# Optimization experiments

Hardware: AMD Instinct MI355X
Metric: run time of the kernel (lower is better)

The kernel has to match this reference:

```python
import jax, jax.numpy as jnp
import numpy as np
from jax import lax

KS = 5            # patch kernel size
STRIDE = 4        # patch stride / scale ratio
SHIFTS = (2, 2)   # roll shifts before patch extraction
SOFTMAX_SCALE = 10.0
MID_CH = 64
BAND_HS = 8


def same_pad(x, k, s):
    """TensorFlow-style SAME padding for kernel k, stride s (NCHW)."""
    H, W = x.shape[-2], x.shape[-1]
    oh, ow = -(-H // s), -(-W // s)
    ph = max(0, (oh - 1) * s + k - H)
    pw = max(0, (ow - 1) * s + k - W)
    return jnp.pad(x, ((0, 0), (0, 0), (ph // 2, ph - ph // 2), (pw // 2, pw - pw // 2)))


def extract_patches(x, k, s, shifts):
    """torch.nn.Unfold equivalent with SAME padding and roll -> [N, L, C, k, k]."""
    x = same_pad(x, k, s)
    x = jnp.roll(x, shifts[0], axis=2)
    x = jnp.roll(x, shifts[1], axis=3)
    p = lax.conv_general_dilated_patches(
        x, (k, k), (s, s), 'VALID', dimension_numbers=('NCHW', 'OIHW', 'NCHW'))
    N, _, Hn, Wn = p.shape
    C = x.shape[1]
    # channel ordering is (C, kh, kw) channel-slowest, matching torch unfold
    return p.reshape(N, C, k, k, Hn * Wn).transpose(0, 4, 1, 2, 3)


def conv3(x, w, b):
    """3x3 conv, padding=1, bias + LeakyReLU(0.01) (BasicBlock)."""
    y = lax.conv_general_dilated(x, w, (1, 1), [(1, 1), (1, 1)],
                                 dimension_numbers=('NCHW', 'OIHW', 'NCHW'))
    return jax.nn.leaky_relu(y + b[None, :, None, None], 0.01)


def setup_inputs() -> dict:
    key = jax.random.key(0)
    ks = jax.random.split(key, 11)
    f32 = jnp.float32
    return {
        'ms':   jax.random.normal(ks[0], (2, BAND_HS, 96, 96), f32),
        'pan':  jax.random.normal(ks[1], (2, 1, 384, 384), f32),
        'pan2': jax.random.normal(ks[2], (2, 1, 96, 96), f32),
        'wq': jax.random.normal(ks[3], (MID_CH, 1, 3, 3), f32) * 0.1,
        'bq': jax.random.normal(ks[4], (MID_CH,), f32) * 0.02,
        'wk': jax.random.normal(ks[5], (MID_CH, 1, 3, 3), f32) * 0.1,
        'bk': jax.random.normal(ks[6], (MID_CH,), f32) * 0.02,
        'wv': jax.random.normal(ks[7], (BAND_HS, BAND_HS, 3, 3), f32) * 0.1,
        'bv': jax.random.normal(ks[8], (BAND_HS,), f32) * 0.02,
        'wr': jax.random.normal(ks[9], (BAND_HS, BAND_HS, 3, 3), f32) * 0.1,
        'br': jax.random.normal(ks[10], (BAND_HS,), f32) * 0.02,
    }


def reference(ms, pan, pan2, wq, bq, wk, bk, wv, bv, wr, br):
    k_fea = conv3(pan2, wk, bk)                       # [N, mid, h, w]
    q_fea = conv3(pan, wq, bq)                        # [N, mid, H, W]
    v_fea = conv3(ms, wv, bv)                         # [N, band, h, w]

    k_patch = extract_patches(k_fea, KS, STRIDE, SHIFTS)  # [N, L, mid, ks, ks]
    v_patch = extract_patches(v_fea, KS, STRIDE, SHIFTS)  # [N, L, band, ks, ks]

    def attend(q, kp, vp):
        # q: [mid, H, W]; kp: [L, mid, ks, ks]; vp: [L, band, ks, ks]
        norms = jnp.sqrt(jnp.sum(kp * kp, axis=(1, 2, 3)))      # per-patch L2 norms
        k0 = kp / jnp.max(norms)                                # global-max normalization
        q0 = same_pad(q[None], KS, STRIDE)                      # [1, mid, Hp, Wp]
        scores = lax.conv_general_dilated(
            q0, k0, (STRIDE, STRIDE), 'VALID',
            dimension_numbers=('NCHW', 'OIHW', 'NCHW'))          # [1, L, H', W']
        attn = jax.nn.softmax(scores * SOFTMAX_SCALE, axis=1)
        # conv_transpose2d(attn, vp, stride) == dilated conv with flipped, transposed kernel
        wT = jnp.flip(vp, (2, 3)).transpose(1, 0, 2, 3)          # [band, L, ks, ks]
        out = lax.conv_general_dilated(
            attn, wT, (1, 1), [(KS - 1, KS - 1)] * 2,
            lhs_dilation=(STRIDE, STRIDE),
            dimension_numbers=('NCHW', 'OIHW', 'NCHW'))          # [1, band, Ho, Wo]
        return out[0] / 6.0

    res = jax.vmap(attend)(q_fea, k_patch, v_patch)   # [N, band, Ho, Wo]
    return conv3(res, wr, br)
```

## Files before the change

kernel.cpp:

```cpp
#include <hip/hip_runtime.h>
#include <math.h>


typedef _Float16 f16;
typedef _Float16 f16x8 __attribute__((ext_vector_type(8)));
typedef float f32x4 __attribute__((ext_vector_type(4)));

namespace csa {
constexpr int NB   = 2;
constexpr int MID  = 64;
constexpr int BAND = 8;
constexpr int HK   = 96;
constexpr int HQ   = 384;
constexpr int HQP  = 385;
constexpr int XI   = 97;
constexpr int LN   = 24;
constexpr int L    = 576;
constexpr int LP   = 640;
constexpr int PS   = 96 * 96;
constexpr int KDIM = MID * 25;
constexpr int VDIM = BAND * 25;
constexpr int MV   = 256;
constexpr int HO   = 385;
constexpr size_t QPSN = (size_t)4 * HQP * XI * MID;

constexpr int NBQ = (NB * 4 * HQP * XI + 255) / 256;
constexpr int NBC = NB * HK * HK / 256;

constexpr size_t align256(size_t x) { return (x + 255) & ~(size_t)255; }
constexpr size_t OFF_QPS  = 0;
constexpr size_t OFF_KCL  = align256(OFF_QPS + (size_t)NB*QPSN*2);
constexpr size_t OFF_VFEA = align256(OFF_KCL + (size_t)NB*HK*HK*MID*2);
constexpr size_t OFF_N2   = align256(OFF_VFEA + (size_t)NB*BAND*HK*HK*4);
constexpr size_t OFF_SC   = align256(OFF_N2   + (size_t)NB*L*4);
constexpr size_t OFF_KM   = align256(OFF_SC   + 256);
constexpr size_t OFF_VT   = align256(OFF_KM   + (size_t)NB*LP*KDIM*2);
constexpr size_t OFF_ST   = align256(OFF_VT   + (size_t)NB*MV*L*2);
constexpr size_t OFF_AT   = align256(OFF_ST   + (size_t)NB*PS*LP*4);
constexpr size_t OFF_D    = align256(OFF_AT   + (size_t)NB*PS*L*2);
}
using namespace csa;

__device__ __forceinline__ void dev_convq(
    const float* __restrict__ in, const float* __restrict__ w,
    const float* __restrict__ b, f16* __restrict__ out, int id) {
  int total = NB * 4 * HQP * XI;
  if (id >= total) return;
  int xi = id % XI;
  int t = id / XI;
  int yp = t % HQP;
  t /= HQP;
  int f = t % 4;
  int n = t / 4;
  int xp = 4 * xi + f;
  f16* op = out + (size_t)id * MID;
  if (yp >= HQ || xp >= HQ) {
    f16x8 z = {0, 0, 0, 0, 0, 0, 0, 0};
#pragma unroll
    for (int c8 = 0; c8 < 8; ++c8) *(f16x8*)(op + c8 * 8) = z;
    return;
  }
  const float* ip = in + (size_t)n * HQ * HQ;
  float p[9];
#pragma unroll
  for (int dy = 0; dy < 3; ++dy)
#pragma unroll
    for (int dx = 0; dx < 3; ++dx) {
      int yy = yp + dy - 1, xx = xp + dx - 1;
      p[dy * 3 + dx] = (yy >= 0 && yy < HQ && xx >= 0 && xx < HQ)
                           ? ip[(size_t)yy * HQ + xx] : 0.f;
    }
#pragma unroll
  for (int c8 = 0; c8 < 8; ++c8) {
    f16x8 o;
#pragma unroll
    for (int e = 0; e < 8; ++e) {
      int co = c8 * 8 + e;
      float acc = b[co];
#pragma unroll
      for (int k = 0; k < 9; ++k) acc = fmaf(p[k], w[co * 9 + k], acc);
      o[e] = (f16)(acc > 0.f ? acc : 0.01f * acc);
    }
    *(f16x8*)(op + c8 * 8) = o;
  }
}

__device__ __forceinline__ void dev_conv_cl(
    const float* __restrict__ in, const float* __restrict__ w,
    const float* __restrict__ b, f16* __restrict__ out, int H, int id) {
  int total = NB * H * H;
  if (id >= total) return;
  int x = id % H;
  int t = id / H;
  int y = t % H;
  int n = t / H;
  f16* op = out + (size_t)id * MID;
  const float* ip = in + (size_t)n * H * H;
  float p[9];
#pragma unroll
  for (int dy = 0; dy < 3; ++dy)
#pragma unroll
    for (int dx = 0; dx < 3; ++dx) {
      int yy = y + dy - 1, xx = x + dx - 1;
      p[dy * 3 + dx] = (yy >= 0 && yy < H && xx >= 0 && xx < H)
                           ? ip[(size_t)yy * H + xx] : 0.f;
    }
#pragma unroll
  for (int c8 = 0; c8 < 8; ++c8) {
    f16x8 o;
#pragma unroll
    for (int e = 0; e < 8; ++e) {
      int co = c8 * 8 + e;
      float acc = b[co];
#pragma unroll
      for (int k = 0; k < 9; ++k) acc = fmaf(p[k], w[co * 9 + k], acc);
      o[e] = (f16)(acc > 0.f ? acc : 0.01f * acc);
    }
    *(f16x8*)(op + c8 * 8) = o;
  }
}

__device__ __forceinline__ void dev_conv8x8(
    const float* __restrict__ in, const float* __restrict__ w,
    const float* __restrict__ b, float* __restrict__ out, int H, int W,
    int id) {
  int total = NB * H * W;
  if (id >= total) return;
  int x = id % W;
  int t = id / W;
  int y = t % H;
  int n = t / H;
  const float* ip = in + (size_t)n * BAND * H * W;
  float p[BAND][9];
#pragma unroll
  for (int ci = 0; ci < BAND; ++ci)
#pragma unroll
    for (int dy = 0; dy < 3; ++dy)
#pragma unroll
      for (int dx = 0; dx < 3; ++dx) {
        int yy = y + dy - 1, xx = x + dx - 1;
        p[ci][dy * 3 + dx] = (yy >= 0 && yy < H && xx >= 0 && xx < W)
                                 ? ip[((size_t)ci * H + yy) * W + xx] : 0.f;
      }
  float* op = out + ((size_t)n * BAND * H + y) * W + x;
  for (int co = 0; co < BAND; ++co) {
    float acc = b[co];
#pragma unroll
    for (int ci = 0; ci < BAND; ++ci)
#pragma unroll
      for (int k = 0; k < 9; ++k)
        acc = fmaf(p[ci][k], w[(co * BAND + ci) * 9 + k], acc);
    acc = acc > 0.f ? acc : 0.01f * acc;
    op[(size_t)co * H * W] = acc;
  }
}

__global__ __launch_bounds__(256) void csa_convs(
    const float* __restrict__ pan, const float* __restrict__ wq,
    const float* __restrict__ bq, f16* __restrict__ qps,
    const float* __restrict__ pan2, const float* __restrict__ wk,
    const float* __restrict__ bk, f16* __restrict__ kcl,
    const float* __restrict__ ms, const float* __restrict__ wv,
    const float* __restrict__ bv, float* __restrict__ v_fea) {
  const int bid = blockIdx.x;
  const int tid = threadIdx.x;
  if (bid < NBQ) {
    dev_convq(pan, wq, bq, qps, bid * 256 + tid);
  } else if (bid < NBQ + NBC) {
    dev_conv_cl(pan2, wk, bk, kcl, HK, (bid - NBQ) * 256 + tid);
  } else {
    dev_conv8x8(ms, wv, bv, v_fea, HK, HK, (bid - NBQ - NBC) * 256 + tid);
  }
}

__global__ __launch_bounds__(256) void csa_build_patches(
    const f16* __restrict__ kcl, const float* __restrict__ v_fea,
    f16* __restrict__ Kmat, f16* __restrict__ Vt, float* __restrict__ n2) {
  int blk = blockIdx.x;
  int n = blk / LP;
  int l = blk % LP;
  int tid = threadIdx.x;
  f16* krow = Kmat + ((size_t)n * LP + l) * KDIM;
  if (l >= L) {
    f16x8 z = {0, 0, 0, 0, 0, 0, 0, 0};
    for (int ch = tid; ch < 200; ch += 256) *(f16x8*)(krow + ch * 8) = z;
    return;
  }
  int i = l / LN, j = l % LN;
  const f16* kn = kcl + (size_t)n * HK * HK * MID;
  float ss = 0.f;
  for (int ch = tid; ch < 200; ch += 256) {
    int khkw = ch >> 3;
    int c0 = (ch & 7) * 8;
    int kh = khkw / 5, kw = khkw % 5;
    int r = (4 * i + kh + 95) % 97;
    int cc = (4 * j + kw + 95) % 97;
    f16x8 v = {0, 0, 0, 0, 0, 0, 0, 0};
    if (r < HK && cc < HK)
      v = *(const f16x8*)(kn + ((size_t)r * HK + cc) * MID + c0);
#pragma unroll
    for (int e = 0; e < 8; ++e) {
      float fv = (float)v[e];
      ss += fv * fv;
    }
    *(f16x8*)(krow + ch * 8) = v;
  }
  for (int m = tid; m < MV; m += 256) {
    float v = 0.f;
    if (m < VDIM) {
      int kw = m % 5;
      int t = m / 5;
      int kh = t % 5;
      int c = t / 5;
      int r = (4 * i + kh + 95) % 97;
      int cc = (4 * j + kw + 95) % 97;
      v = (r < HK && cc < HK)
              ? v_fea[(((size_t)n * BAND + c) * HK + r) * HK + cc] : 0.f;
    }
    Vt[((size_t)n * MV + m) * L + l] = (f16)v;
  }
  __shared__ float red[256];
  red[tid] = ss;
  __syncthreads();
  for (int s = 128; s > 0; s >>= 1) {
    if (tid < s) red[tid] += red[tid + s];
    __syncthreads();
  }
  if (tid == 0) n2[n * L + l] = red[0];
}

__global__ __launch_bounds__(256) void csa_max_scale(
    const float* __restrict__ n2, float* __restrict__ scale) {
  int n = blockIdx.x;
  int tid = threadIdx.x;
  float m = 0.f;
  for (int l = tid; l < L; l += 256) m = fmaxf(m, n2[n * L + l]);
  __shared__ float red[256];
  red[tid] = m;
  __syncthreads();
  for (int s = 128; s > 0; s >>= 1) {
    if (tid < s) red[tid] = fmaxf(red[tid], red[tid + s]);
    __syncthreads();
  }
  if (tid == 0) scale[n] = 10.f / sqrtf(red[0]);
}

__device__ __forceinline__ void gl_lds16(const f16* g, f16* s) {
  __builtin_amdgcn_global_load_lds(
      (const __attribute__((address_space(1))) void*)g,
      (__attribute__((address_space(3))) void*)s, 16, 0, 0);
}

__global__ __launch_bounds__(256) void csa_gemm1(
    const f16* __restrict__ qps, const f16* __restrict__ Km,
    float* __restrict__ C) {
  __shared__ __attribute__((aligned(16))) f16 As[3 * 4096];
  __shared__ __attribute__((aligned(16))) f16 Bs[3 * 4096];
  const int tid = threadIdx.x;
  const int w = tid >> 6;
  const int l = tid & 63;
  const int q = l >> 4;
  const int r = l & 15;

  const int flat = blockIdx.x + 5 * (blockIdx.y + 72 * blockIdx.z);
  const int logical = (flat & 7) * 90 + (flat >> 3);
  const int bx = logical % 5;
  const int by = (logical / 5) % 72;
  const int nb = logical / 360;

  qps += (size_t)nb * QPSN;
  Km += (size_t)nb * LP * KDIM;
  C += (size_t)nb * (size_t)PS * L;
  const int bm = by * 128;
  const int bn = bx * 128;
  const int wm = (w >> 1) * 64;
  const int wn = (w & 1) * 64;

  f32x4 acc[4][4];
#pragma unroll
  for (int i = 0; i < 4; ++i)
#pragma unroll
    for (int j = 0; j < 4; ++j) {
      f32x4 z = {0.f, 0.f, 0.f, 0.f};
      acc[i][j] = z;
    }

  const int pg0 = bm + w * 16;
  const int y0 = pg0 / 96, x0 = pg0 % 96;
  const int pg1 = pg0 + 64;
  const int y1 = pg1 / 96, x1 = pg1 % 96;
  const int la = r * MID + q * 8;

  const f16* gb0 = Km + (size_t)(bn + w * 16 + r) * KDIM + q * 8;
  const f16* gb1 = gb0 + (size_t)64 * KDIM;
  const int am = (w >> 1) * 4;
  const int bnn = (w & 1) * 4;

  auto stage = [&](int t, int bi) {
    f16* bA = As + bi * 4096;
    f16* bB = Bs + bi * 4096;
    const int kh = t / 10;
    const int rem = t - kh * 10;
    const int kw = rem >> 1;
    const int half = rem & 1;
    const size_t u0 =
        (((size_t)(kw & 3) * HQP + (4 * y0 + kh)) * XI + x0 + (kw >> 2)) * MID;
    const size_t u1 =
        (((size_t)(kw & 3) * HQP + (4 * y1 + kh)) * XI + x1 + (kw >> 2)) * MID;
    const size_t oA = (size_t)half * 32 + la;
    gl_lds16(qps + u0 + oA, bA + w * 512);
    gl_lds16(qps + u1 + oA, bA + 2048 + w * 512);
    gl_lds16(gb0 + (size_t)t * 32, bB + w * 512);
    gl_lds16(gb1 + (size_t)t * 32, bB + 2048 + w * 512);
  };
  auto compute = [&](int bi) {
    const f16* bA = As + bi * 4096;
    const f16* bB = Bs + bi * 4096;
    f16x8 af[4], bf[4];
#pragma unroll
    for (int u = 0; u < 4; ++u) {
      af[u] = *(const f16x8*)&bA[(am + u) * 512 + q * 128 + r * 8];
      bf[u] = *(const f16x8*)&bB[(bnn + u) * 512 + q * 128 + r * 8];
    }
#pragma unroll
    for (int i = 0; i < 4; ++i)
#pragma unroll
      for (int j = 0; j < 4; ++j)
        acc[i][j] = __builtin_amdgcn_mfma_f32_16x16x32_f16(af[i], bf[j],
                                                           acc[i][j], 0, 0, 0);
  };

  stage(0, 0);
  stage(1, 1);
  int bi = 0;
  for (int t = 0; t < 48; ++t) {
    asm volatile("s_waitcnt vmcnt(4)" ::: "memory");
    __builtin_amdgcn_s_barrier();
    __builtin_amdgcn_sched_barrier(0);
    stage(t + 2, bi == 0 ? 2 : bi - 1);
    compute(bi);
    bi = (bi == 2) ? 0 : bi + 1;
  }
  asm volatile("s_waitcnt vmcnt(4)" ::: "memory");
  __builtin_amdgcn_s_barrier();
  __builtin_amdgcn_sched_barrier(0);
  compute(bi);
  bi = (bi == 2) ? 0 : bi + 1;
  asm volatile("s_waitcnt vmcnt(0)" ::: "memory");
  __builtin_amdgcn_s_barrier();
  __builtin_amdgcn_sched_barrier(0);
  compute(bi);

  const int cn = bn + wn + r;
#pragma unroll
  for (int i = 0; i < 4; ++i) {
    int rm = bm + wm + i * 16 + q * 4;
#pragma unroll
    for (int j = 0; j < 4; ++j) {
      int c = cn + j * 16;
      if (c < L) {
#pragma unroll
        for (int rr = 0; rr < 4; ++rr)
          C[(size_t)(rm + rr) * L + c] = acc[i][j][rr];
      }
    }
  }
}

__global__ __launch_bounds__(256) void csa_gemm2(
    const f16* __restrict__ Vt, const f16* __restrict__ At,
    float* __restrict__ D) {
  __shared__ __attribute__((aligned(16))) f16 As[3 * 2048];
  __shared__ __attribute__((aligned(16))) f16 Bs[3 * 4096];
  const int tid = threadIdx.x;
  const int w = tid >> 6;
  const int l = tid & 63;
  const int q = l >> 4;
  const int r = l & 15;

  const int flat = blockIdx.x + 72 * (blockIdx.y + 4 * blockIdx.z);
  const int logical = (flat & 7) * 72 + (flat >> 3);
  const int nx = logical % 72;
  const int my = (logical / 72) % 4;
  const int nb = logical / 288;

  const f16* A = Vt + (size_t)nb * MV * L;
  const f16* Bt = At + (size_t)nb * (size_t)PS * L;
  float* C = D + (size_t)nb * (size_t)MV * PS;
  const int bm = my * 64;
  const int bn = nx * 128;
  const int wm = (w >> 1) * 32;
  const int wn = (w & 1) * 64;

  f32x4 acc[2][4];
#pragma unroll
  for (int i = 0; i < 2; ++i)
#pragma unroll
    for (int j = 0; j < 4; ++j) {
      f32x4 z = {0.f, 0.f, 0.f, 0.f};
      acc[i][j] = z;
    }

  const f16* ga  = A + (size_t)(bm + w * 16 + r) * L + q * 8;
  const f16* gb0 = Bt + (size_t)(bn + w * 16 + r) * L + q * 8;
  const f16* gb1 = gb0 + (size_t)64 * L;
  const int am = (w >> 1) * 2;
  const int bnn = (w & 1) * 4;

  auto stage = [&](int t, int bi) {
    f16* bA = As + bi * 2048;
    f16* bB = Bs + bi * 4096;
    const size_t k0 = (size_t)t * 32;
    gl_lds16(ga + k0, bA + w * 512);
    gl_lds16(gb0 + k0, bB + w * 512);
    gl_lds16(gb1 + k0, bB + 2048 + w * 512);
  };
  auto compute = [&](int bi) {
    const f16* bA = As + bi * 2048;
    const f16* bB = Bs + bi * 4096;
    f16x8 af[2], bf[4];
#pragma unroll
    for (int u = 0; u < 2; ++u)
      af[u] = *(const f16x8*)&bA[(am + u) * 512 + q * 128 + r * 8];
#pragma unroll
    for (int u = 0; u < 4; ++u)
      bf[u] = *(const f16x8*)&bB[(bnn + u) * 512 + q * 128 + r * 8];
#pragma unroll
    for (int i = 0; i < 2; ++i)
#pragma unroll
      for (int j = 0; j < 4; ++j)
        acc[i][j] = __builtin_amdgcn_mfma_f32_16x16x32_f16(af[i], bf[j],
                                                           acc[i][j], 0, 0, 0);
  };

  stage(0, 0);
  stage(1, 1);
  int bi = 0;
  for (int t = 0; t < 16; ++t) {
    asm volatile("s_waitcnt vmcnt(3)" ::: "memory");
    __builtin_amdgcn_s_barrier();
    __builtin_amdgcn_sched_barrier(0);
    stage(t + 2, bi == 0 ? 2 : bi - 1);
    compute(bi);
    bi = (bi == 2) ? 0 : bi + 1;
  }
  asm volatile("s_waitcnt vmcnt(3)" ::: "memory");
  __builtin_amdgcn_s_barrier();
  __builtin_amdgcn_sched_barrier(0);
  compute(bi);
  bi = (bi == 2) ? 0 : bi + 1;
  asm volatile("s_waitcnt vmcnt(0)" ::: "memory");
  __builtin_amdgcn_s_barrier();
  __builtin_amdgcn_sched_barrier(0);
  compute(bi);

  const int cn = bn + wn + r;
#pragma unroll
  for (int i = 0; i < 2; ++i) {
    int rm = bm + wm + i * 16 + q * 4;
#pragma unroll
    for (int j = 0; j < 4; ++j)
#pragma unroll
      for (int rr = 0; rr < 4; ++rr)
        C[(size_t)(rm + rr) * PS + cn + j * 16] = acc[i][j][rr];
  }
}

__global__ __launch_bounds__(256) void csa_softmax(
    const float* __restrict__ scoresT, const float* __restrict__ scale,
    f16* __restrict__ attnT) {
  const int wv = threadIdx.x >> 6;
  const int lane = threadIdx.x & 63;
  const int p = blockIdx.x * 4 + wv;
  const int n = blockIdx.y;
  const float sc = scale[n];
  const float* row = scoresT + ((size_t)n * PS + p) * L;
  float v[9];
  float m = -1e30f;
#pragma unroll
  for (int j = 0; j < 9; ++j) {
    v[j] = row[lane + j * 64] * sc;
    m = fmaxf(m, v[j]);
  }
#pragma unroll
  for (int off = 32; off > 0; off >>= 1) m = fmaxf(m, __shfl_xor(m, off));
  float e[9], s = 0.f;
#pragma unroll
  for (int j = 0; j < 9; ++j) {
    e[j] = __expf(v[j] - m);
    s += e[j];
  }
#pragma unroll
  for (int off = 32; off > 0; off >>= 1) s += __shfl_xor(s, off);
  const float inv = 1.f / s;
  f16* orow = attnT + ((size_t)n * PS + p) * L;
#pragma unroll
  for (int j = 0; j < 9; ++j) orow[lane + j * 64] = (f16)(e[j] * inv);
}

__global__ __launch_bounds__(256) void csa_gather_conv(
    const float* __restrict__ D, const float* __restrict__ wr,
    const float* __restrict__ br, float* __restrict__ out) {
  __shared__ float rs[BAND][18][18];
  __shared__ float wsm[BAND * BAND * 9];
  __shared__ float brs[BAND];
  const int tid = threadIdx.x;
  const int n = blockIdx.z;
  const int ty = blockIdx.y, tx = blockIdx.x;
  const float* Dn = D + (size_t)n * MV * PS;

  for (int i = tid; i < BAND * BAND * 9; i += 256) wsm[i] = wr[i];
  if (tid < BAND) brs[tid] = br[tid];

  for (int idx = tid; idx < BAND * 18 * 18; idx += 256) {
    int ci = idx / 324;
    int rem = idx - ci * 324;
    int yy = rem / 18;
    int xx = rem - yy * 18;
    int oy = ty * 16 - 1 + yy;
    int ox = tx * 16 - 1 + xx;
    float s = 0.f;
    if (oy >= 0 && oy < HO && ox >= 0 && ox < HO) {
      int kh0 = oy & 3;
      int kw0 = ox & 3;
      for (int kh = kh0; kh < 5; kh += 4) {
        int y = (oy - kh) >> 2;
        if (y < 0 || y >= 96) continue;
        for (int kw = kw0; kw < 5; kw += 4) {
          int x = (ox - kw) >> 2;
          if (x < 0 || x >= 96) continue;
          s += Dn[(size_t)(ci * 25 + kh * 5 + kw) * PS + y * 96 + x];
        }
      }
      s *= (1.f / 6.f);
    }
    rs[ci][yy][xx] = s;
  }
  __syncthreads();

  const int y = tid >> 4, x = tid & 15;
  const int oy = ty * 16 + y, ox = tx * 16 + x;
  if (oy >= HO || ox >= HO) return;
  float p[BAND][9];
#pragma unroll
  for (int ci = 0; ci < BAND; ++ci)
#pragma unroll
    for (int dy = 0; dy < 3; ++dy)
#pragma unroll
      for (int dx = 0; dx < 3; ++dx)
        p[ci][dy * 3 + dx] = rs[ci][y + dy][x + dx];
  float* op = out + ((size_t)n * BAND * HO + oy) * HO + ox;
  for (int co = 0; co < BAND; ++co) {
    float acc = brs[co];
#pragma unroll
    for (int ci = 0; ci < BAND; ++ci)
#pragma unroll
      for (int k = 0; k < 9; ++k)
        acc = fmaf(p[ci][k], wsm[(co * BAND + ci) * 9 + k], acc);
    acc = acc > 0.f ? acc : 0.01f * acc;
    op[(size_t)co * HO * HO] = acc;
  }
}

extern "C" void kernel_launch(void* const* d_in, const int* in_sizes, int n_in,
                              void* d_out, int out_size, void* d_ws,
                              size_t ws_size, hipStream_t stream) {
  const float* ms   = (const float*)d_in[0];
  const float* pan  = (const float*)d_in[1];
  const float* pan2 = (const float*)d_in[2];
  const float* wq = (const float*)d_in[3];
  const float* bq = (const float*)d_in[4];
  const float* wk = (const float*)d_in[5];
  const float* bk = (const float*)d_in[6];
  const float* wv = (const float*)d_in[7];
  const float* bv = (const float*)d_in[8];
  const float* wr = (const float*)d_in[9];
  const float* br = (const float*)d_in[10];
  float* out = (float*)d_out;

  char* ws = (char*)d_ws;
  f16*   qps   = (f16*)(ws + OFF_QPS);
  f16*   kcl   = (f16*)(ws + OFF_KCL);
  float* v_fea = (float*)(ws + OFF_VFEA);
  float* n2    = (float*)(ws + OFF_N2);
  float* scale = (float*)(ws + OFF_SC);
  f16*   Kmat  = (f16*)(ws + OFF_KM);
  f16*   Vt    = (f16*)(ws + OFF_VT);
  float* scoT  = (float*)(ws + OFF_ST);
  f16*   attnT = (f16*)(ws + OFF_AT);
  float* Dm    = (float*)(ws + OFF_D);

  dim3 b256(256);
  csa_convs<<<dim3(NBQ + 2 * NBC), b256, 0, stream>>>(
      pan, wq, bq, qps, pan2, wk, bk, kcl, ms, wv, bv, v_fea);
  csa_build_patches<<<dim3(NB * LP), b256, 0, stream>>>(kcl, v_fea, Kmat, Vt,
                                                        n2);
  csa_max_scale<<<dim3(NB), b256, 0, stream>>>(n2, scale);

  csa_gemm1<<<dim3(LP / 128, PS / 128, NB), b256, 0, stream>>>(qps, Kmat,
                                                               scoT);

  csa_softmax<<<dim3(PS / 4, NB), b256, 0, stream>>>(scoT, scale, attnT);

  csa_gemm2<<<dim3(PS / 128, MV / 64, NB), b256, 0, stream>>>(Vt, attnT, Dm);

  csa_gather_conv<<<dim3((HO + 15) / 16, (HO + 15) / 16, NB), b256, 0,
                    stream>>>(Dm, wr, br, out);
}
```

Before: 274.3 us.

## Restructure score GEMM to 8 waves with double-buffered 64-wide K stages

The first attention GEMM now runs 512 threads (8 waves) per 128x128 tile, each wave owning a 32x64 sub-tile, instead of 4 waves owning 64x64. The K loop moves from 48 triple-buffered 32-wide steps to 24 double-buffered 64-wide steps, each split into two MFMA phases and raising wave priority around the MFMA block. The intent is more waves to hide LDS and global-to-LDS latency with fewer barriers per K element. The trade-off is an extra barrier per iteration to protect the double buffer, and fewer registers available per thread under the new launch bounds.

```diff
diff --git a/kernel.cpp b/kernel.cpp
--- a/kernel.cpp
+++ b/kernel.cpp
@@ -251,11 +251,11 @@
       (__attribute__((address_space(3))) void*)s, 16, 0, 0);
 }
 
-__global__ __launch_bounds__(256) void csa_gemm1(
+__global__ __launch_bounds__(512, 4) void csa_gemm1(
     const f16* __restrict__ qps, const f16* __restrict__ Km,
     float* __restrict__ C) {
-  __shared__ __attribute__((aligned(16))) f16 As[3 * 4096];
-  __shared__ __attribute__((aligned(16))) f16 Bs[3 * 4096];
+  __shared__ __attribute__((aligned(16))) f16 As[2][8192];
+  __shared__ __attribute__((aligned(16))) f16 Bs[2][8192];
   const int tid = threadIdx.x;
   const int w = tid >> 6;
   const int l = tid & 63;
@@ -273,12 +273,12 @@
   C += (size_t)nb * (size_t)PS * L;
   const int bm = by * 128;
   const int bn = bx * 128;
-  const int wm = (w >> 1) * 64;
-  const int wn = (w & 1) * 64;
-
-  f32x4 acc[4][4];
-#pragma unroll
-  for (int i = 0; i < 4; ++i)
+  const int wmw = (w >> 1) * 32;
+  const int wnw = (w & 1) * 64;
+
+  f32x4 acc[2][4];
+#pragma unroll
+  for (int i = 0; i < 2; ++i)
 #pragma unroll
     for (int j = 0; j < 4; ++j) {
       f32x4 z = {0.f, 0.f, 0.f, 0.f};
@@ -287,81 +287,74 @@
 
   const int pg0 = bm + w * 16;
   const int y0 = pg0 / 96, x0 = pg0 % 96;
-  const int pg1 = pg0 + 64;
-  const int y1 = pg1 / 96, x1 = pg1 % 96;
   const int la = r * MID + q * 8;
-
-  const f16* gb0 = Km + (size_t)(bn + w * 16 + r) * KDIM + q * 8;
-  const f16* gb1 = gb0 + (size_t)64 * KDIM;
-  const int am = (w >> 1) * 4;
-  const int bnn = (w & 1) * 4;
-
-  auto stage = [&](int t, int bi) {
-    f16* bA = As + bi * 4096;
-    f16* bB = Bs + bi * 4096;
-    const int kh = t / 10;
-    const int rem = t - kh * 10;
-    const int kw = rem >> 1;
-    const int half = rem & 1;
+  const f16* gb = Km + (size_t)(bn + w * 16 + r) * KDIM + q * 8;
+
+  auto stage = [&](int t, int c) {
+    const int kh = t / 5, kw = t - kh * 5;
     const size_t u0 =
-        (((size_t)(kw & 3) * HQP + (4 * y0 + kh)) * XI + x0 + (kw >> 2)) * MID;
-    const size_t u1 =
-        (((size_t)(kw & 3) * HQP + (4 * y1 + kh)) * XI + x1 + (kw >> 2)) * MID;
-    const size_t oA = (size_t)half * 32 + la;
-    gl_lds16(qps + u0 + oA, bA + w * 512);
-    gl_lds16(qps + u1 + oA, bA + 2048 + w * 512);
-    gl_lds16(gb0 + (size_t)t * 32, bB + w * 512);
-    gl_lds16(gb1 + (size_t)t * 32, bB + 2048 + w * 512);
+        (((size_t)(kw & 3) * HQP + (4 * y0 + kh)) * XI + x0 + (kw >> 2)) * MID +
+        la;
+    const f16* gk = gb + (size_t)t * 64;
+    f16* dA = &As[c][(w * 2) * 512];
+    f16* dB = &Bs[c][(w * 2) * 512];
+    gl_lds16(qps + u0, dA);
+    gl_lds16(qps + u0 + 32, dA + 512);
+    gl_lds16(gk, dB);
+    gl_lds16(gk + 32, dB + 512);
   };
-  auto compute = [&](int bi) {
-    const f16* bA = As + bi * 4096;
-    const f16* bB = Bs + bi * 4096;
-    f16x8 af[4], bf[4];
-#pragma unroll
-    for (int u = 0; u < 4; ++u) {
-      af[u] = *(const f16x8*)&bA[(am + u) * 512 + q * 128 + r * 8];
-      bf[u] = *(const f16x8*)&bB[(bnn + u) * 512 + q * 128 + r * 8];
-    }
-#pragma unroll
-    for (int i = 0; i < 4; ++i)
+
+  const int ag = (w >> 1) * 2;
+  const int bg = (w & 1) * 4;
+  const int lo = q * 128 + r * 8;
+  auto phase = [&](int c, int kk) {
+    f16x8 af[2], bf[4];
+#pragma unroll
+    for (int u = 0; u < 2; ++u)
+      af[u] = *(const f16x8*)&As[c][((ag + u) * 2 + kk) * 512 + lo];
+#pragma unroll
+    for (int j = 0; j < 4; ++j)
+      bf[j] = *(const f16x8*)&Bs[c][((bg + j) * 2 + kk) * 512 + lo];
+    __builtin_amdgcn_s_setprio(1);
+#pragma unroll
+    for (int i = 0; i < 2; ++i)
 #pragma unroll
       for (int j = 0; j < 4; ++j)
         acc[i][j] = __builtin_amdgcn_mfma_f32_16x16x32_f16(af[i], bf[j],
                                                            acc[i][j], 0, 0, 0);
+    __builtin_amdgcn_s_setprio(0);
   };
 
   stage(0, 0);
   stage(1, 1);
-  int bi = 0;
-  for (int t = 0; t < 48; ++t) {
+  for (int t = 0; t < 24; ++t) {
+    const int c = t & 1;
     asm volatile("s_waitcnt vmcnt(4)" ::: "memory");
     __builtin_amdgcn_s_barrier();
     __builtin_amdgcn_sched_barrier(0);
-    stage(t + 2, bi == 0 ? 2 : bi - 1);
-    compute(bi);
-    bi = (bi == 2) ? 0 : bi + 1;
-  }
-  asm volatile("s_waitcnt vmcnt(4)" ::: "memory");
-  __builtin_amdgcn_s_barrier();
-  __builtin_amdgcn_sched_barrier(0);
-  compute(bi);
-  bi = (bi == 2) ? 0 : bi + 1;
+    phase(c, 0);
+    phase(c, 1);
+    __builtin_amdgcn_sched_barrier(0);
+    __builtin_amdgcn_s_barrier();
+    if (t < 23) stage(t + 2, c);
+  }
   asm volatile("s_waitcnt vmcnt(0)" ::: "memory");
   __builtin_amdgcn_s_barrier();
   __builtin_amdgcn_sched_barrier(0);
-  compute(bi);
-
-  const int cn = bn + wn + r;
-#pragma unroll
-  for (int i = 0; i < 4; ++i) {
-    int rm = bm + wm + i * 16 + q * 4;
+  phase(0, 0);
+  phase(0, 1);
+
+  const int cn = bn + wnw + r;
+#pragma unroll
+  for (int i = 0; i < 2; ++i) {
+    int rm = bm + wmw + i * 16 + q * 4;
 #pragma unroll
     for (int j = 0; j < 4; ++j) {
-      int c = cn + j * 16;
-      if (c < L) {
+      int cc = cn + j * 16;
+      if (cc < L) {
 #pragma unroll
         for (int rr = 0; rr < 4; ++rr)
-          C[(size_t)(rm + rr) * L + c] = acc[i][j][rr];
+          C[(size_t)(rm + rr) * L + cc] = acc[i][j][rr];
       }
     }
   }
@@ -597,8 +590,8 @@
                                                         n2);
   csa_max_scale<<<dim3(NB), b256, 0, stream>>>(n2, scale);
 
-  csa_gemm1<<<dim3(LP / 128, PS / 128, NB), b256, 0, stream>>>(qps, Kmat,
-                                                               scoT);
+  csa_gemm1<<<dim3(LP / 128, PS / 128, NB), dim3(512), 0, stream>>>(qps, Kmat,
+                                                                    scoT);
 
   csa_softmax<<<dim3(PS / 4, NB), b256, 0, stream>>>(scoT, scale, attnT);
 
```

Measured after the change: 282.5 us. 3.0% more time.
